# Kernel tuning notes

Measured on AMD Instinct MI355X. Metric: run time of the kernel, lower is better.

The kernel has to match this reference:

```python
import jax, jax.numpy as jnp
import numpy as np

B, S, D, H = 2, 2048, 1024, 16
DK = D // H
NEG = -65504.0  # matches torch masked_fill value in source


def setup_inputs() -> dict:
    key = jax.random.key(0)
    ks = jax.random.split(key, 5)
    scale = 1.0 / np.sqrt(D)
    return {
        "x": jax.random.normal(ks[0], (B, S, D), dtype=jnp.float32),
        "W_q": jax.random.normal(ks[1], (D, D), dtype=jnp.float32) * scale,
        "W_k": jax.random.normal(ks[2], (D, D), dtype=jnp.float32) * scale,
        "W_v": jax.random.normal(ks[3], (D, D), dtype=jnp.float32) * scale,
        "W_o": jax.random.normal(ks[4], (D, D), dtype=jnp.float32) * scale,
    }


def reference(x, W_q, W_k, W_v, W_o):
    b, s, d = x.shape
    # nn.Linear(x) = x @ W.T ; split heads -> [b, h, s, dk]
    def proj(W):
        return (x @ W.T).reshape(b, s, H, DK).transpose(0, 2, 1, 3)
    q, k, v = proj(W_q), proj(W_k), proj(W_v)
    scores = jnp.einsum("bhqd,bhkd->bhqk", q, k) / jnp.sqrt(jnp.float32(DK))
    causal = jnp.tril(jnp.ones((s, s), dtype=bool))  # True where attending allowed
    scores = jnp.where(causal, scores, NEG)
    attn = jax.nn.softmax(scores, axis=-1)  # attn_pdrop=0 -> dropout is identity
    out = jnp.einsum("bhqk,bhkd->bhqd", attn, v)
    out = out.transpose(0, 2, 1, 3).reshape(b, s, d)
    return out @ W_o.T
```

## Files before the change

kernel.cpp:

```cpp
#include <hip/hip_runtime.h>
#include <hip/hip_bf16.h>

typedef __attribute__((ext_vector_type(4))) float f32x4;
typedef __attribute__((ext_vector_type(8))) short bf16x8;

#define Bn 2
#define Sn 2048
#define Dn 1024
#define Hn 16
#define DKn 64
#define Mrows (Bn * Sn)

__device__ __forceinline__ unsigned short f2bf(float f) {
  unsigned int x = __float_as_uint(f);
  x += 0x7fffu + ((x >> 16) & 1u);
  return (unsigned short)(x >> 16);
}

__device__ __forceinline__ float bf2f(unsigned short u) {
  return __uint_as_float(((unsigned int)u) << 16);
}

__device__ __forceinline__ unsigned int cvtpk(float lo, float hi) {
  unsigned int r;
  asm("v_cvt_pk_bf16_f32 %0, %1, %2" : "=v"(r) : "v"(lo), "v"(hi));
  return r;
}

__device__ __forceinline__ float exp2a(float x) {
  float r;
  asm("v_exp_f32 %0, %1" : "=v"(r) : "v"(x));
  return r;
}

__device__ __forceinline__ f32x4 mfma16(bf16x8 a, bf16x8 b, f32x4 c) {
  return __builtin_amdgcn_mfma_f32_16x16x32_bf16(a, b, c, 0, 0, 0);
}

__device__ __forceinline__ f32x4 max4(f32x4 a, f32x4 b) {
  f32x4 r;
  r[0] = fmaxf(a[0], b[0]); r[1] = fmaxf(a[1], b[1]);
  r[2] = fmaxf(a[2], b[2]); r[3] = fmaxf(a[3], b[3]);
  return r;
}

__device__ __forceinline__ void gload_lds16(const unsigned short* g, unsigned short* l) {
  __builtin_amdgcn_global_load_lds(
      (const __attribute__((address_space(1))) void*)g,
      (__attribute__((address_space(3))) void*)l, 16, 0, 0);
}

__global__ __launch_bounds__(256)
void cvt_all(const float* __restrict__ x,  const float* __restrict__ wq,
             const float* __restrict__ wk, const float* __restrict__ wv,
             const float* __restrict__ wo,
             unsigned short* __restrict__ xb,  unsigned short* __restrict__ wqb,
             unsigned short* __restrict__ wkb, unsigned short* __restrict__ wvb,
             unsigned short* __restrict__ wob) {
  int i = (blockIdx.x * 256 + threadIdx.x) * 4;
  const float* src; unsigned short* dst; int off;
  int r = i >> 20;
  if (r < 4)       { src = x;  dst = xb;  off = i; }
  else if (r == 4) { src = wq; dst = wqb; off = i & 1048575; }
  else if (r == 5) { src = wk; dst = wkb; off = i & 1048575; }
  else if (r == 6) { src = wv; dst = wvb; off = i & 1048575; }
  else             { src = wo; dst = wob; off = i & 1048575; }
  float4 v = *(const float4*)(src + off);
  ushort4 o;
  o.x = f2bf(v.x); o.y = f2bf(v.y); o.z = f2bf(v.z); o.w = f2bf(v.w);
  *(ushort4*)(dst + off) = o;
}

template<int MODE>
__device__ __forceinline__ void gemm_body(const unsigned short* __restrict__ A,
                                          const unsigned short* __restrict__ W,
                                          unsigned short* __restrict__ Cb,
                                          float* __restrict__ Cf,
                                          unsigned short* As,
                                          unsigned short* Bs) {
  const int K = Dn, N = Dn;
  const int tid  = threadIdx.x;
  const int wid  = tid >> 6;
  const int lane = tid & 63;
  const int l15  = lane & 15;
  const int lg   = lane >> 4;
  const int row0 = blockIdx.x * 128;
  const int col0 = blockIdx.y * 128;
  const int wr = (wid >> 1) * 64;
  const int wc = (wid & 1) * 64;

  f32x4 acc[4][4] = {};

  const int lrow2 = lane >> 2;
  const int gs    = (lane & 3) ^ ((lane >> 3) & 3);
  const int swzr  = (l15 >> 1) & 3;

  auto stage = [&](int kt, int b) {
#pragma unroll
    for (int q = 0; q < 2; ++q) {
      int chunk = wid * 2 + q;
      int r = chunk * 16 + lrow2;
      gload_lds16(A + (size_t)(row0 + r) * K + kt + gs * 8,
                  &As[b * 4096 + chunk * 512]);
    }
#pragma unroll
    for (int q = 0; q < 2; ++q) {
      int chunk = wid * 2 + q;
      int r = chunk * 16 + lrow2;
      gload_lds16(W + (size_t)(col0 + r) * K + kt + gs * 8,
                  &Bs[b * 4096 + chunk * 512]);
    }
  };

  auto compute = [&](int b) {
    bf16x8 af[4], bfr[4];
#pragma unroll
    for (int m = 0; m < 4; ++m)
      af[m] = *(const bf16x8*)(&As[b * 4096 + (wr + m * 16 + l15) * 32 +
                                   ((lg ^ swzr) * 8)]);
#pragma unroll
    for (int n = 0; n < 4; ++n)
      bfr[n] = *(const bf16x8*)(&Bs[b * 4096 + (wc + n * 16 + l15) * 32 +
                                    ((lg ^ swzr) * 8)]);
    __builtin_amdgcn_s_setprio(1);
#pragma unroll
    for (int m = 0; m < 4; ++m)
#pragma unroll
      for (int n = 0; n < 4; ++n)
        acc[m][n] = mfma16(af[m], bfr[n], acc[m][n]);
    __builtin_amdgcn_s_setprio(0);
  };

  stage(0, 0);
  stage(32, 1);
  int cb = 0;
#pragma unroll 1
  for (int t = 0; t < 32; ++t) {
    if (t < 31) asm volatile("s_waitcnt vmcnt(4)" ::: "memory");
    else        asm volatile("s_waitcnt vmcnt(0)" ::: "memory");
    __builtin_amdgcn_sched_barrier(0);
    __builtin_amdgcn_s_barrier();
    __builtin_amdgcn_sched_barrier(0);
    if (t <= 29) {
      int sb = cb + 2; if (sb >= 3) sb -= 3;
      stage((t + 2) * 32, sb);
    }
    compute(cb);
    ++cb; if (cb == 3) cb = 0;
  }

#pragma unroll
  for (int m = 0; m < 4; ++m)
#pragma unroll
    for (int n = 0; n < 4; ++n) {
      int r0 = row0 + wr + m * 16 + lg * 4;
      int c  = col0 + wc + n * 16 + l15;
      if (MODE == 2) {
        int b = r0 >> 11, s = r0 & 2047;
        int h = c >> 6,  d = c & 63;
        ushort4 pw;
        pw.x = f2bf(acc[m][n][0]); pw.y = f2bf(acc[m][n][1]);
        pw.z = f2bf(acc[m][n][2]); pw.w = f2bf(acc[m][n][3]);
        *(ushort4*)(Cb + ((((size_t)b * Hn + h) * DKn + d) << 11) + s) = pw;
      } else {
#pragma unroll
        for (int j = 0; j < 4; ++j) {
          size_t idx = (size_t)(r0 + j) * N + c;
          float v = acc[m][n][j];
          if (MODE == 3)      Cf[idx] = v;
          else if (MODE == 0) Cb[idx] = f2bf(v * 0.18033688f);
          else                Cb[idx] = f2bf(v);
        }
      }
    }
}

__global__ __launch_bounds__(256, 3)
void gemm_qkv(const unsigned short* __restrict__ A,
              const unsigned short* __restrict__ W0,
              const unsigned short* __restrict__ W1,
              const unsigned short* __restrict__ W2,
              unsigned short* __restrict__ C0,
              unsigned short* __restrict__ C1,
              unsigned short* __restrict__ C2) {
  __shared__ unsigned short As[3 * 128 * 32];
  __shared__ unsigned short Bs[3 * 128 * 32];
  if (blockIdx.z == 0)      gemm_body<0>(A, W0, C0, nullptr, As, Bs);
  else if (blockIdx.z == 1) gemm_body<1>(A, W1, C1, nullptr, As, Bs);
  else                      gemm_body<2>(A, W2, C2, nullptr, As, Bs);
}

__global__ __launch_bounds__(256, 3)
void gemm_out(const unsigned short* __restrict__ A,
              const unsigned short* __restrict__ W,
              float* __restrict__ C) {
  __shared__ unsigned short As[3 * 128 * 32];
  __shared__ unsigned short Bs[3 * 128 * 32];
  gemm_body<3>(A, W, nullptr, C, As, Bs);
}

__global__ __launch_bounds__(256, 3)
void attn_part(const unsigned short* __restrict__ Qg,
               const unsigned short* __restrict__ Kg,
               const unsigned short* __restrict__ Vtg,
               unsigned short* __restrict__ Og,
               unsigned short* __restrict__ Pb,
               float* __restrict__ Pml) {
  const int bid = blockIdx.x;
  const int bh = bid & 31;
  const int j  = bid >> 5;
  const int bb = bh >> 4, hh = bh & 15;
  const int tid = threadIdx.x, wid = tid >> 6, lane = tid & 63;
  const int l15 = lane & 15, lg = lane >> 4;
  const int wq = wid * 32;
  const size_t baseQ = (size_t)bb * Sn * Dn + (size_t)hh * DKn;
  const size_t baseV = (size_t)bh * DKn * Sn;

  __shared__ unsigned short Ks[2][64 * 64];
  __shared__ unsigned short Vts[2][64 * 64];
  __shared__ unsigned short Ps[4][32 * 72];

  const int lrow  = lane >> 3;
  const int sgran = (lane & 7) ^ lrow;
  const int swz   = l15 & 7;

  const int bstart = (34 * j) / 3;
  const int nt = (34 * (j + 1)) / 3 - bstart;

  int qt = 0;
  while ((qt + 1) * (qt + 2) <= bstart) ++qt;
  int kt = bstart - qt * (qt + 1);

  int sqt = qt, skt = kt;
  auto stage = [&](int t, int b) {
    const int k0 = t << 6;
#pragma unroll
    for (int p = 0; p < 2; ++p) {
      int c = p * 4 + wid;
      int r = c * 8 + lrow;
      gload_lds16(Kg + baseQ + (size_t)(k0 + r) * Dn + sgran * 8, &Ks[b][c * 512]);
    }
#pragma unroll
    for (int p = 0; p < 2; ++p) {
      int c = p * 4 + wid;
      int dr = c * 8 + lrow;
      gload_lds16(Vtg + baseV + (size_t)dr * Sn + k0 + sgran * 8, &Vts[b][c * 512]);
    }
  };
  auto advs = [&]() { ++skt; if (skt == 2 * sqt + 2) { skt = 0; ++sqt; } };

  stage(skt, 0); advs();
  __syncthreads();

  bf16x8 qf[2][2];
  auto loadQ = [&](int qtile) {
    const int q0 = qtile * 128;
#pragma unroll
    for (int qm = 0; qm < 2; ++qm)
#pragma unroll
      for (int kd = 0; kd < 2; ++kd)
        qf[qm][kd] = *(const bf16x8*)(Qg + baseQ +
                     (size_t)(q0 + wq + qm * 16 + l15) * Dn + kd * 32 + lg * 8);
  };
  loadQ(qt);

  f32x4 oacc[2][4] = {};
  float mrun[2] = {-1e30f, -1e30f};
  float lrun[2] = {0.f, 0.f};
  int pstart = kt;

  for (int i = 0; i < nt; ++i) {
    const int cur = i & 1;
    if (i < nt - 1) { stage(skt, cur ^ 1); advs(); }
    const int k0 = kt << 6;
    const int q0 = qt * 128;

    if (k0 <= q0 + wq + 31) {
      f32x4 sf[2][4] = {};
      __builtin_amdgcn_s_setprio(1);
#pragma unroll
      for (int kn = 0; kn < 4; ++kn)
#pragma unroll
        for (int kd = 0; kd < 2; ++kd) {
          bf16x8 kf = *(const bf16x8*)(&Ks[cur][(kn * 16 + l15) * 64 +
                                              (((kd * 4 + lg) ^ swz) * 8)]);
          sf[0][kn] = mfma16(kf, qf[0][kd], sf[0][kn]);
          sf[1][kn] = mfma16(kf, qf[1][kd], sf[1][kn]);
        }
      __builtin_amdgcn_s_setprio(0);

      if (k0 + 63 > q0 + wq) {
#pragma unroll
        for (int qm = 0; qm < 2; ++qm) {
          int qq = q0 + wq + qm * 16 + l15;
#pragma unroll
          for (int kn = 0; kn < 4; ++kn)
#pragma unroll
            for (int jj = 0; jj < 4; ++jj) {
              int key = k0 + kn * 16 + lg * 4 + jj;
              if (key > qq) sf[qm][kn][jj] = -1e30f;
            }
        }
      }

#pragma unroll
      for (int qm = 0; qm < 2; ++qm) {
        f32x4 mm = max4(max4(sf[qm][0], sf[qm][1]), max4(sf[qm][2], sf[qm][3]));
        float tl = fmaxf(fmaxf(mm[0], mm[1]), fmaxf(mm[2], mm[3]));
        if (__any(tl > mrun[qm] + 11.5f)) {
          float t = tl;
          t = fmaxf(t, __shfl_xor(t, 16));
          t = fmaxf(t, __shfl_xor(t, 32));
          float mnew = fmaxf(mrun[qm], t);
          float corr = exp2a(mrun[qm] - mnew);
          mrun[qm] = mnew;
          lrun[qm] *= corr;
#pragma unroll
          for (int dn = 0; dn < 4; ++dn) oacc[qm][dn] *= corr;
        }
        const float m = mrun[qm];
#pragma unroll
        for (int kn = 0; kn < 4; ++kn) {
#pragma unroll
          for (int jj = 0; jj < 4; ++jj)
            sf[qm][kn][jj] = exp2a(sf[qm][kn][jj] - m);
          uint2 pw;
          pw.x = cvtpk(sf[qm][kn][0], sf[qm][kn][1]);
          pw.y = cvtpk(sf[qm][kn][2], sf[qm][kn][3]);
          *(uint2*)(&Ps[wid][(qm * 16 + l15) * 72 + kn * 16 + lg * 4]) = pw;
        }
        f32x4 sv = (sf[qm][0] + sf[qm][1]) + (sf[qm][2] + sf[qm][3]);
        lrun[qm] += (sv[0] + sv[1]) + (sv[2] + sv[3]);
      }

      __builtin_amdgcn_s_setprio(1);
#pragma unroll
      for (int kk = 0; kk < 2; ++kk) {
        bf16x8 pf[2];
#pragma unroll
        for (int qm = 0; qm < 2; ++qm)
          pf[qm] = *(const bf16x8*)(&Ps[wid][(qm * 16 + l15) * 72 + kk * 32 + lg * 8]);
#pragma unroll
        for (int dn = 0; dn < 4; ++dn) {
          bf16x8 vf = *(const bf16x8*)(&Vts[cur][(dn * 16 + l15) * 64 +
                                               (((kk * 4 + lg) ^ swz) * 8)]);
#pragma unroll
          for (int qm = 0; qm < 2; ++qm)
            oacc[qm][dn] = mfma16(vf, pf[qm], oacc[qm][dn]);
        }
      }
      __builtin_amdgcn_s_setprio(0);
    }

    const bool segend = (kt == 2 * qt + 1);
    if (segend || i == nt - 1) {
      if (pstart == 0 && segend) {
#pragma unroll
        for (int qm = 0; qm < 2; ++qm) {
          float lt = lrun[qm];
          lt += __shfl_xor(lt, 16);
          lt += __shfl_xor(lt, 32);
          float rinv = 1.0f / lt;
          int row = q0 + wq + qm * 16 + l15;
#pragma unroll
          for (int dn = 0; dn < 4; ++dn) {
            ushort4 ow;
            ow.x = f2bf(oacc[qm][dn][0] * rinv);
            ow.y = f2bf(oacc[qm][dn][1] * rinv);
            ow.z = f2bf(oacc[qm][dn][2] * rinv);
            ow.w = f2bf(oacc[qm][dn][3] * rinv);
            *(ushort4*)(Og + baseQ + (size_t)row * Dn + dn * 16 + lg * 4) = ow;
          }
        }
      } else {
        const size_t slot = (size_t)bh * 40 + (pstart == 0 ? qt : 16 + j);
#pragma unroll
        for (int qm = 0; qm < 2; ++qm) {
          float lt = lrun[qm];
          lt += __shfl_xor(lt, 16);
          lt += __shfl_xor(lt, 32);
          int rl = wq + qm * 16 + l15;
#pragma unroll
          for (int dn = 0; dn < 4; ++dn) {
            ushort4 ow;
            ow.x = f2bf(oacc[qm][dn][0]);
            ow.y = f2bf(oacc[qm][dn][1]);
            ow.z = f2bf(oacc[qm][dn][2]);
            ow.w = f2bf(oacc[qm][dn][3]);
            *(ushort4*)(Pb + slot * 8192 + (size_t)rl * 64 + dn * 16 + lg * 4) = ow;
          }
          if (lg == 0) {
            Pml[slot * 256 + rl] = mrun[qm];
            Pml[slot * 256 + 128 + rl] = lt;
          }
        }
      }
      if (i < nt - 1) {
        ++qt; kt = 0; pstart = 0;
        loadQ(qt);
#pragma unroll
        for (int qm = 0; qm < 2; ++qm) {
          mrun[qm] = -1e30f; lrun[qm] = 0.f;
#pragma unroll
          for (int dn = 0; dn < 4; ++dn) oacc[qm][dn] = f32x4{0.f, 0.f, 0.f, 0.f};
        }
      }
    } else {
      ++kt;
    }
    __syncthreads();
  }
}

__global__ __launch_bounds__(256)
void attn_combine(const unsigned short* __restrict__ Pb,
                  const float* __restrict__ Pml,
                  unsigned short* __restrict__ Og) {
  const int b = blockIdx.x;
  const int bh = b >> 4, qt = b & 15;
  const int s = qt * (qt + 1);
  const int e = s + 2 * qt + 2;
  const int js = (3 * s + 2) / 34;
  const int je = (3 * (e - 1) + 2) / 34;
  const int np = je - js + 1;
  if (np == 1) return;
  const int bb = bh >> 4, hh = bh & 15;
  const size_t baseQ = (size_t)bb * Sn * Dn + (size_t)hh * DKn;
  const int q0 = qt * 128;
  const int r = threadIdx.x >> 1;
  const int c32 = (threadIdx.x & 1) * 32;

  const size_t s0 = (size_t)bh * 40 + qt;
  const size_t s1 = (size_t)bh * 40 + 16 + js + 1;
  const size_t s2 = (size_t)bh * 40 + 16 + js + 2;
  const size_t s3 = (size_t)bh * 40 + 16 + js + 3;

  float m0 = Pml[s0 * 256 + r],      l0 = Pml[s0 * 256 + 128 + r];
  float m1 = Pml[s1 * 256 + r],      l1 = Pml[s1 * 256 + 128 + r];
  float m2 = -1e30f, l2 = 0.f, m3 = -1e30f, l3 = 0.f;
  if (np > 2) { m2 = Pml[s2 * 256 + r]; l2 = Pml[s2 * 256 + 128 + r]; }
  if (np > 3) { m3 = Pml[s3 * 256 + r]; l3 = Pml[s3 * 256 + 128 + r]; }

  float M = fmaxf(fmaxf(m0, m1), fmaxf(m2, m3));
  float w0 = exp2a(m0 - M), w1 = exp2a(m1 - M);
  float w2 = (np > 2) ? exp2a(m2 - M) : 0.f;
  float w3 = (np > 3) ? exp2a(m3 - M) : 0.f;
  float L = l0 * w0 + l1 * w1 + l2 * w2 + l3 * w3;

  float acc[32];
#pragma unroll
  for (int k = 0; k < 32; ++k) acc[k] = 0.f;

  auto accum = [&](size_t slot, float w) {
    const unsigned short* src = Pb + slot * 8192 + (size_t)r * 64 + c32;
#pragma unroll
    for (int k4 = 0; k4 < 8; ++k4) {
      ushort4 v = *(const ushort4*)(src + k4 * 4);
      acc[k4 * 4 + 0] += w * bf2f(v.x);
      acc[k4 * 4 + 1] += w * bf2f(v.y);
      acc[k4 * 4 + 2] += w * bf2f(v.z);
      acc[k4 * 4 + 3] += w * bf2f(v.w);
    }
  };
  accum(s0, w0);
  accum(s1, w1);
  if (np > 2) accum(s2, w2);
  if (np > 3) accum(s3, w3);

  float rinv = 1.0f / L;
#pragma unroll
  for (int k4 = 0; k4 < 8; ++k4) {
    ushort4 o;
    o.x = f2bf(acc[k4 * 4 + 0] * rinv);
    o.y = f2bf(acc[k4 * 4 + 1] * rinv);
    o.z = f2bf(acc[k4 * 4 + 2] * rinv);
    o.w = f2bf(acc[k4 * 4 + 3] * rinv);
    *(ushort4*)(Og + baseQ + (size_t)(q0 + r) * Dn + c32 + k4 * 4) = o;
  }
}

extern "C" void kernel_launch(void* const* d_in, const int* in_sizes, int n_in,
                              void* d_out, int out_size, void* d_ws, size_t ws_size,
                              hipStream_t stream) {
  const float* x  = (const float*)d_in[0];
  const float* Wq = (const float*)d_in[1];
  const float* Wk = (const float*)d_in[2];
  const float* Wv = (const float*)d_in[3];
  const float* Wo = (const float*)d_in[4];
  float* out = (float*)d_out;

  char* ws = (char*)d_ws;
  size_t off = 0;
  unsigned short* xb  = (unsigned short*)(ws + off); off += (size_t)Mrows * Dn * 2;
  unsigned short* wqb = (unsigned short*)(ws + off); off += (size_t)Dn * Dn * 2;
  unsigned short* wkb = (unsigned short*)(ws + off); off += (size_t)Dn * Dn * 2;
  unsigned short* wvb = (unsigned short*)(ws + off); off += (size_t)Dn * Dn * 2;
  unsigned short* wob = (unsigned short*)(ws + off); off += (size_t)Dn * Dn * 2;
  unsigned short* Qb  = (unsigned short*)(ws + off); off += (size_t)Mrows * Dn * 2;
  unsigned short* Kb  = (unsigned short*)(ws + off); off += (size_t)Mrows * Dn * 2;
  unsigned short* Vtb = (unsigned short*)(ws + off); off += (size_t)Mrows * Dn * 2;
  unsigned short* Ob  = (unsigned short*)(ws + off); off += (size_t)Mrows * Dn * 2;
  unsigned short* Pb  = (unsigned short*)(ws + off); off += (size_t)1280 * 8192 * 2;
  float*          Pml = (float*)(ws + off);          off += (size_t)1280 * 256 * 4;

  cvt_all<<<8192, 256, 0, stream>>>(x, Wq, Wk, Wv, Wo, xb, wqb, wkb, wvb, wob);
  gemm_qkv<<<dim3(Mrows / 128, Dn / 128, 3), 256, 0, stream>>>(xb, wqb, wkb, wvb, Qb, Kb, Vtb);
  attn_part<<<768, 256, 0, stream>>>(Qb, Kb, Vtb, Ob, Pb, Pml);
  attn_combine<<<512, 256, 0, stream>>>(Pb, Pml, Ob);
  gemm_out<<<dim3(Mrows / 128, Dn / 128), 256, 0, stream>>>(Ob, wob, out);
}
```

Measured before the change: 109.8 us.

## Split attention work into more chunks and load V fragments directly from global

Raises the attention grid from 768 to 1024 blocks with 8.5 tile-steps per block instead of about 11.3, and increases launch bounds to 4 waves per SIMD. It drops the shared-memory staging of V^T and instead loads V fragments from global memory into registers before the softmax. The partial-slot stride grows to 48, and the combine kernel becomes a generic loop over partials. The aim is better load balance and occupancy with less LDS use. The cost is uncoalesced global V reads without double buffering and more partials to combine.

New measurement: 160.8 us. +46.6%, slower.

```diff
diff --git a/kernel.cpp b/kernel.cpp
--- a/kernel.cpp
+++ b/kernel.cpp
@@ -199,7 +199,7 @@
   gemm_body<3>(A, W, nullptr, C, As, Bs);
 }
 
-__global__ __launch_bounds__(256, 3)
+__global__ __launch_bounds__(256, 4)
 void attn_part(const unsigned short* __restrict__ Qg,
                const unsigned short* __restrict__ Kg,
                const unsigned short* __restrict__ Vtg,
@@ -217,15 +217,14 @@
   const size_t baseV = (size_t)bh * DKn * Sn;
 
   __shared__ unsigned short Ks[2][64 * 64];
-  __shared__ unsigned short Vts[2][64 * 64];
   __shared__ unsigned short Ps[4][32 * 72];
 
   const int lrow  = lane >> 3;
   const int sgran = (lane & 7) ^ lrow;
   const int swz   = l15 & 7;
 
-  const int bstart = (34 * j) / 3;
-  const int nt = (34 * (j + 1)) / 3 - bstart;
+  const int bstart = (17 * j) >> 1;
+  const int nt = ((17 * (j + 1)) >> 1) - bstart;
 
   int qt = 0;
   while ((qt + 1) * (qt + 2) <= bstart) ++qt;
@@ -239,12 +238,6 @@
       int c = p * 4 + wid;
       int r = c * 8 + lrow;
       gload_lds16(Kg + baseQ + (size_t)(k0 + r) * Dn + sgran * 8, &Ks[b][c * 512]);
-    }
-#pragma unroll
-    for (int p = 0; p < 2; ++p) {
-      int c = p * 4 + wid;
-      int dr = c * 8 + lrow;
-      gload_lds16(Vtg + baseV + (size_t)dr * Sn + k0 + sgran * 8, &Vts[b][c * 512]);
     }
   };
   auto advs = [&]() { ++skt; if (skt == 2 * sqt + 2) { skt = 0; ++sqt; } };
@@ -288,6 +281,14 @@
           sf[1][kn] = mfma16(kf, qf[1][kd], sf[1][kn]);
         }
       __builtin_amdgcn_s_setprio(0);
+
+      bf16x8 vf[2][4];
+#pragma unroll
+      for (int kk = 0; kk < 2; ++kk)
+#pragma unroll
+        for (int dn = 0; dn < 4; ++dn)
+          vf[kk][dn] = *(const bf16x8*)(Vtg + baseV +
+                       (size_t)(dn * 16 + l15) * Sn + k0 + kk * 32 + lg * 8);
 
       if (k0 + 63 > q0 + wq) {
 #pragma unroll
@@ -341,13 +342,10 @@
         for (int qm = 0; qm < 2; ++qm)
           pf[qm] = *(const bf16x8*)(&Ps[wid][(qm * 16 + l15) * 72 + kk * 32 + lg * 8]);
 #pragma unroll
-        for (int dn = 0; dn < 4; ++dn) {
-          bf16x8 vf = *(const bf16x8*)(&Vts[cur][(dn * 16 + l15) * 64 +
-                                               (((kk * 4 + lg) ^ swz) * 8)]);
+        for (int dn = 0; dn < 4; ++dn)
 #pragma unroll
           for (int qm = 0; qm < 2; ++qm)
-            oacc[qm][dn] = mfma16(vf, pf[qm], oacc[qm][dn]);
-        }
+            oacc[qm][dn] = mfma16(vf[kk][dn], pf[qm], oacc[qm][dn]);
       }
       __builtin_amdgcn_s_setprio(0);
     }
@@ -373,7 +371,7 @@
           }
         }
       } else {
-        const size_t slot = (size_t)bh * 40 + (pstart == 0 ? qt : 16 + j);
+        const size_t slot = (size_t)bh * 48 + (pstart == 0 ? qt : 16 + j);
 #pragma unroll
         for (int qm = 0; qm < 2; ++qm) {
           float lt = lrun[qm];
@@ -420,8 +418,8 @@
   const int bh = b >> 4, qt = b & 15;
   const int s = qt * (qt + 1);
   const int e = s + 2 * qt + 2;
-  const int js = (3 * s + 2) / 34;
-  const int je = (3 * (e - 1) + 2) / 34;
+  const int js = (2 * s + 1) / 17;
+  const int je = (2 * (e - 1) + 1) / 17;
   const int np = je - js + 1;
   if (np == 1) return;
   const int bb = bh >> 4, hh = bh & 15;
@@ -430,28 +428,20 @@
   const int r = threadIdx.x >> 1;
   const int c32 = (threadIdx.x & 1) * 32;
 
-  const size_t s0 = (size_t)bh * 40 + qt;
-  const size_t s1 = (size_t)bh * 40 + 16 + js + 1;
-  const size_t s2 = (size_t)bh * 40 + 16 + js + 2;
-  const size_t s3 = (size_t)bh * 40 + 16 + js + 3;
-
-  float m0 = Pml[s0 * 256 + r],      l0 = Pml[s0 * 256 + 128 + r];
-  float m1 = Pml[s1 * 256 + r],      l1 = Pml[s1 * 256 + 128 + r];
-  float m2 = -1e30f, l2 = 0.f, m3 = -1e30f, l3 = 0.f;
-  if (np > 2) { m2 = Pml[s2 * 256 + r]; l2 = Pml[s2 * 256 + 128 + r]; }
-  if (np > 3) { m3 = Pml[s3 * 256 + r]; l3 = Pml[s3 * 256 + 128 + r]; }
-
-  float M = fmaxf(fmaxf(m0, m1), fmaxf(m2, m3));
-  float w0 = exp2a(m0 - M), w1 = exp2a(m1 - M);
-  float w2 = (np > 2) ? exp2a(m2 - M) : 0.f;
-  float w3 = (np > 3) ? exp2a(m3 - M) : 0.f;
-  float L = l0 * w0 + l1 * w1 + l2 * w2 + l3 * w3;
-
+  float M = -1e30f;
+  for (int p = 0; p < np; ++p) {
+    size_t slot = (size_t)bh * 48 + (p == 0 ? qt : 16 + js + p);
+    M = fmaxf(M, Pml[slot * 256 + r]);
+  }
+
+  float L = 0.f;
   float acc[32];
 #pragma unroll
   for (int k = 0; k < 32; ++k) acc[k] = 0.f;
-
-  auto accum = [&](size_t slot, float w) {
+  for (int p = 0; p < np; ++p) {
+    size_t slot = (size_t)bh * 48 + (p == 0 ? qt : 16 + js + p);
+    float w = exp2a(Pml[slot * 256 + r] - M);
+    L += Pml[slot * 256 + 128 + r] * w;
     const unsigned short* src = Pb + slot * 8192 + (size_t)r * 64 + c32;
 #pragma unroll
     for (int k4 = 0; k4 < 8; ++k4) {
@@ -461,11 +451,7 @@
       acc[k4 * 4 + 2] += w * bf2f(v.z);
       acc[k4 * 4 + 3] += w * bf2f(v.w);
     }
-  };
-  accum(s0, w0);
-  accum(s1, w1);
-  if (np > 2) accum(s2, w2);
-  if (np > 3) accum(s3, w3);
+  }
 
   float rinv = 1.0f / L;
 #pragma unroll
@@ -500,12 +486,12 @@
   unsigned short* Kb  = (unsigned short*)(ws + off); off += (size_t)Mrows * Dn * 2;
   unsigned short* Vtb = (unsigned short*)(ws + off); off += (size_t)Mrows * Dn * 2;
   unsigned short* Ob  = (unsigned short*)(ws + off); off += (size_t)Mrows * Dn * 2;
-  unsigned short* Pb  = (unsigned short*)(ws + off); off += (size_t)1280 * 8192 * 2;
-  float*          Pml = (float*)(ws + off);          off += (size_t)1280 * 256 * 4;
+  unsigned short* Pb  = (unsigned short*)(ws + off); off += (size_t)32 * 48 * 8192 * 2;
+  float*          Pml = (float*)(ws + off);          off += (size_t)32 * 48 * 256 * 4;
 
   cvt_all<<<8192, 256, 0, stream>>>(x, Wq, Wk, Wv, Wo, xb, wqb, wkb, wvb, wob);
   gemm_qkv<<<dim3(Mrows / 128, Dn / 128, 3), 256, 0, stream>>>(xb, wqb, wkb, wvb, Qb, Kb, Vtb);
-  attn_part<<<768, 256, 0, stream>>>(Qb, Kb, Vtb, Ob, Pb, Pml);
+  attn_part<<<1024, 256, 0, stream>>>(Qb, Kb, Vtb, Ob, Pb, Pml);
   attn_combine<<<512, 256, 0, stream>>>(Pb, Pml, Ob);
   gemm_out<<<dim3(Mrows / 128, Dn / 128), 256, 0, stream>>>(Ob, wob, out);
 }
```
